# Performance work log

Measured on AMD Instinct MI355X. Metric: run time of the kernel, lower is better.

The kernel has to match this reference:

```python
import jax, jax.numpy as jnp
import numpy as np

B, S, F, H = 4, 1024, 512, 16
D = F // H  # head_dim = 32

def setup_inputs() -> dict:
    key = jax.random.key(0)
    ks = jax.random.split(key, 9)
    init = lambda k, shp: 0.1 * jax.random.normal(k, shp, dtype=jnp.float32)
    return {
        "kv": jax.random.normal(ks[0], (B, S, F), dtype=jnp.float32),
        "q": jax.random.normal(ks[1], (B, S, F), dtype=jnp.float32),
        "mask": jnp.ones((B, 1, S, S), dtype=jnp.int32),
        "Wq": init(ks[2], (F, F)),
        "Wk": init(ks[3], (F, F)),
        "Wv": init(ks[4], (F, F)),
        "Wo": init(ks[5], (F, F)),
        "rel_table": init(ks[6], (2 * S + 1, D)),  # nn.Embed(2*length_q+1, head_dim)
        "Wrel": init(ks[7], (D, D)),  # rel_pos_dense, no bias
    }

def reference(kv, q, mask, Wq, Wk, Wv, Wo, rel_table, Wrel):
    b, s, f = q.shape
    h, d = H, f // H
    qh = (q @ Wq).reshape(b, s, h, d)
    kh = (kv @ Wk).reshape(b, s, h, d)
    vh = (kv @ Wv).reshape(b, s, h, d)
    # raw content scores [b,h,q,k]
    scores = jnp.einsum('bqhd,bkhd->bhqk', qh, kh)
    # relative-position embedding: dist in [0, 2s], table lookup + dense
    dist = jnp.arange(s)[None, :] - jnp.arange(s)[:, None] + s  # [q,k]
    emb = rel_table[dist] @ Wrel  # [q,k,d]
    scores = scores + jnp.einsum('bqhd,qkd->bhqk', qh, emb)
    scores = scores / jnp.sqrt(jnp.asarray(d, scores.dtype))
    # mask-select before softmax (mask [b,1,q,k] broadcast over heads)
    scores = jnp.where(mask > 0, scores, -jnp.inf)
    attn = jax.nn.softmax(scores, axis=-1)
    out = jnp.einsum('bhqk,bkhd->bqhd', attn, vh).reshape(b, s, f)
    return out @ Wo  # dropout is identity (training=False)
```

## Files before the change

### kernel.cpp

```cpp
#include <hip/hip_runtime.h>

#define S_ 1024
#define H_ 16
#define D_ 32

typedef float f32x4 __attribute__((ext_vector_type(4)));
typedef short bf16x8 __attribute__((ext_vector_type(8)));
typedef unsigned long long u64;

static __device__ __forceinline__ short f2b(float f) {
    union { float f; unsigned u; } x; x.f = f;
    unsigned u = x.u;
    unsigned r = u + 0x7fffu + ((u >> 16) & 1u);
    return (short)(r >> 16);
}
static __device__ __forceinline__ unsigned pk_rne(float lo, float hi) {
    union { float f; unsigned u; } a, b; a.f = lo; b.f = hi;
    unsigned ul = a.u + 0x7fffu + ((a.u >> 16) & 1u);
    unsigned uh = b.u + 0x7fffu + ((b.u >> 16) & 1u);
    return __builtin_amdgcn_perm(uh, ul, 0x07060302u);
}
static __device__ __forceinline__ unsigned pk_trunc(float lo, float hi) {
    union { float f; unsigned u; } a, b; a.f = lo; b.f = hi;
    return __builtin_amdgcn_perm(b.u, a.u, 0x07060302u);
}
static __device__ __forceinline__ float bperm(int bidx, float v) {
    union { float f; int i; } x; x.f = v;
    x.i = __builtin_amdgcn_ds_bpermute(bidx, x.i);
    return x.f;
}
static __device__ __forceinline__ int stg64(int row, int c8) {
    return row * 72 + (c8 ^ ((row & 3) << 3));
}

__global__ __launch_bounds__(256)
void prep_kernel(const float* __restrict__ rt, short* __restrict__ relb,
                 const int* __restrict__ mask, u64* __restrict__ mbits,
                 const float* __restrict__ Wq, const float* __restrict__ Wk,
                 const float* __restrict__ Wv, const float* __restrict__ Wo,
                 short* __restrict__ Wt)
{
    __shared__ float ls[32][33];
    int bid = blockIdx.x, t = threadIdx.x;
    if (bid < 257) {
        int i = bid * 256 + t;
        if (i < 2049 * 32) relb[i] = f2b(rt[i]);
        return;
    }
    bid -= 257;
    if (bid < 4096) {
        #pragma unroll
        for (int j = 0; j < 4; ++j) {
            int i = bid * 1024 + j * 256 + t;
            u64 bal = __ballot(mask[i] > 0);
            if ((t & 63) == 0) mbits[i >> 6] = bal;
        }
        return;
    }
    bid -= 4096;
    int mat = bid >> 8, tl = bid & 255, ti = tl >> 4, tj = tl & 15;
    const float* W = (mat == 0) ? Wq : (mat == 1) ? Wk : (mat == 2) ? Wv : Wo;
    int r = t >> 3, c = (t & 7) * 4;
    float4 v = *(const float4*)(W + (long)(ti * 32 + r) * 512 + tj * 32 + c);
    ls[r][c] = v.x; ls[r][c + 1] = v.y; ls[r][c + 2] = v.z; ls[r][c + 3] = v.w;
    __syncthreads();
    int nl = t >> 3, kk = (t & 7) * 4;
    uint2 o = { pk_rne(ls[kk][nl], ls[kk + 1][nl]),
                pk_rne(ls[kk + 2][nl], ls[kk + 3][nl]) };
    *(uint2*)(Wt + ((long)mat * 512 + tj * 32 + nl) * 512 + ti * 32 + kk) = o;
}

__global__ __launch_bounds__(256)
void gemm3_kernel(const float* __restrict__ q, const float* __restrict__ kv,
                  const short* __restrict__ Wt,
                  short* __restrict__ qh, short* __restrict__ kh, short* __restrict__ vt,
                  float scale)
{
    __shared__ __align__(16) short a_s[64 * 72];
    __shared__ __align__(16) short b_s[64 * 72];
    const int t = threadIdx.x;
    const int w = t >> 6, lane = t & 63, l15 = lane & 15, quad = lane >> 4;
    const int wm = w & 1, wn = w >> 1;

    int bid = blockIdx.x;
    const int mat = bid >> 9;
    const int rr_ = bid & 511;
    const int bm = (rr_ & 63) * 64, bn = (rr_ >> 6) * 64;
    const float* A = (mat == 0) ? q : kv;
    const short* Wm = Wt + (long)mat * 262144;

    const int srow = t >> 2, scg = (t & 3) << 4;
    f32x4 acc[2][2] = {};

    for (int k0 = 0; k0 < 512; k0 += 64) {
        {
            const float* ap = A + (long)(bm + srow) * 512 + k0 + scg;
            float4 v0 = *(const float4*)(ap);
            float4 v1 = *(const float4*)(ap + 4);
            float4 v2 = *(const float4*)(ap + 8);
            float4 v3 = *(const float4*)(ap + 12);
            uint4 o0 = { pk_rne(v0.x, v0.y), pk_rne(v0.z, v0.w),
                         pk_rne(v1.x, v1.y), pk_rne(v1.z, v1.w) };
            uint4 o1 = { pk_rne(v2.x, v2.y), pk_rne(v2.z, v2.w),
                         pk_rne(v3.x, v3.y), pk_rne(v3.z, v3.w) };
            *(uint4*)(a_s + stg64(srow, scg)) = o0;
            *(uint4*)(a_s + stg64(srow, scg + 8)) = o1;
        }
        {
            const short* bp = Wm + (long)(bn + srow) * 512 + k0 + scg;
            *(bf16x8*)(b_s + stg64(srow, scg))     = *(const bf16x8*)(bp);
            *(bf16x8*)(b_s + stg64(srow, scg + 8)) = *(const bf16x8*)(bp + 8);
        }
        __syncthreads();
        bf16x8 af[2][2], bfr[2][2];
        #pragma unroll
        for (int i = 0; i < 2; ++i)
            #pragma unroll
            for (int ks = 0; ks < 2; ++ks) {
                af[i][ks]  = *(const bf16x8*)(a_s + stg64(wm * 32 + i * 16 + l15, ks * 32 + quad * 8));
                bfr[i][ks] = *(const bf16x8*)(b_s + stg64(wn * 32 + i * 16 + l15, ks * 32 + quad * 8));
            }
        if (mat == 2) {
            #pragma unroll
            for (int i = 0; i < 2; ++i)
                #pragma unroll
                for (int j = 0; j < 2; ++j)
                    #pragma unroll
                    for (int ks = 0; ks < 2; ++ks)
                        acc[i][j] = __builtin_amdgcn_mfma_f32_16x16x32_bf16(bfr[i][ks], af[j][ks], acc[i][j], 0, 0, 0);
        } else {
            #pragma unroll
            for (int i = 0; i < 2; ++i)
                #pragma unroll
                for (int j = 0; j < 2; ++j)
                    #pragma unroll
                    for (int ks = 0; ks < 2; ++ks)
                        acc[i][j] = __builtin_amdgcn_mfma_f32_16x16x32_bf16(af[i][ks], bfr[j][ks], acc[i][j], 0, 0, 0);
        }
        __syncthreads();
    }

    if (mat < 2) {
        short* out = (mat == 0) ? qh : kh;
        float alpha = (mat == 0) ? scale : 1.0f;
        #pragma unroll
        for (int i = 0; i < 2; ++i)
            #pragma unroll
            for (int j = 0; j < 2; ++j)
                #pragma unroll
                for (int r = 0; r < 4; ++r) {
                    int m = bm + wm * 32 + i * 16 + quad * 4 + r;
                    int n = bn + wn * 32 + j * 16 + l15;
                    int bb = m >> 10, s = m & 1023, hh = n >> 5, dd = n & 31;
                    out[((long)((bb * 16 + hh) * 1024 + s)) * 32 + dd] = f2b(acc[i][j][r] * alpha);
                }
    } else {
        #pragma unroll
        for (int i = 0; i < 2; ++i)
            #pragma unroll
            for (int j = 0; j < 2; ++j)
                #pragma unroll
                for (int r = 0; r < 4; ++r) {
                    int n = bn + wn * 32 + i * 16 + quad * 4 + r;
                    int m = bm + wm * 32 + j * 16 + l15;
                    int bb = m >> 10, s = m & 1023, hh = n >> 5, dd = n & 31;
                    int sp = (s & ~63) | ((s & 15) << 2) | ((s >> 4) & 3);
                    vt[((long)((bb * 16 + hh) * 32 + dd)) * 1024 + sp] = f2b(acc[i][j][r]);
                }
    }
}

__global__ __launch_bounds__(256)
void gemm_out_kernel(const short* __restrict__ ao, const short* __restrict__ Wt,
                     float* __restrict__ out)
{
    __shared__ __align__(16) short a_s[64 * 72];
    __shared__ __align__(16) short b_s[64 * 72];
    const int t = threadIdx.x;
    const int w = t >> 6, lane = t & 63, l15 = lane & 15, quad = lane >> 4;
    const int wm = w & 1, wn = w >> 1;
    const int bm = (blockIdx.x & 63) * 64, bn = (blockIdx.x >> 6) * 64;
    const short* Wm = Wt + (long)3 * 262144;
    const int srow = t >> 2, scg = (t & 3) << 4;
    f32x4 acc[2][2] = {};

    for (int k0 = 0; k0 < 512; k0 += 64) {
        {
            const short* apb = ao + (long)(bm + srow) * 512 + k0 + scg;
            *(bf16x8*)(a_s + stg64(srow, scg))     = *(const bf16x8*)(apb);
            *(bf16x8*)(a_s + stg64(srow, scg + 8)) = *(const bf16x8*)(apb + 8);
            const short* bpb = Wm + (long)(bn + srow) * 512 + k0 + scg;
            *(bf16x8*)(b_s + stg64(srow, scg))     = *(const bf16x8*)(bpb);
            *(bf16x8*)(b_s + stg64(srow, scg + 8)) = *(const bf16x8*)(bpb + 8);
        }
        __syncthreads();
        bf16x8 af[2][2], bfr[2][2];
        #pragma unroll
        for (int i = 0; i < 2; ++i)
            #pragma unroll
            for (int ks = 0; ks < 2; ++ks) {
                af[i][ks]  = *(const bf16x8*)(a_s + stg64(wm * 32 + i * 16 + l15, ks * 32 + quad * 8));
                bfr[i][ks] = *(const bf16x8*)(b_s + stg64(wn * 32 + i * 16 + l15, ks * 32 + quad * 8));
            }
        #pragma unroll
        for (int i = 0; i < 2; ++i)
            #pragma unroll
            for (int j = 0; j < 2; ++j)
                #pragma unroll
                for (int ks = 0; ks < 2; ++ks)
                    acc[i][j] = __builtin_amdgcn_mfma_f32_16x16x32_bf16(af[i][ks], bfr[j][ks], acc[i][j], 0, 0, 0);
        __syncthreads();
    }
    #pragma unroll
    for (int i = 0; i < 2; ++i)
        #pragma unroll
        for (int j = 0; j < 2; ++j)
            #pragma unroll
            for (int r = 0; r < 4; ++r) {
                int m = bm + wm * 32 + i * 16 + quad * 4 + r;
                int n = bn + wn * 32 + j * 16 + l15;
                out[(long)m * 512 + n] = acc[i][j][r];
            }
}

__global__ __launch_bounds__(256)
void attn_kernel(const short* __restrict__ qh, const float* __restrict__ wrel,
                 const short* __restrict__ kh, const short* __restrict__ vt,
                 const short* __restrict__ relb, const u64* __restrict__ mbits,
                 short* __restrict__ ao)
{
    __shared__ __align__(16) short smem[4 * 2 * 16 * 72];
    const int t = threadIdx.x;
    const int w = t >> 6, lane = t & 63, l15 = lane & 15, quad = lane >> 4;
    short* pw0 = smem + w * (2 * 16 * 72);
    short* pw1 = pw0 + 16 * 72;

    const int half = w & 1, qsel = w >> 1;
    const int gw = blockIdx.x * 2 + qsel;
    const int qt = gw & 63, h = (gw >> 6) & 15, b = gw >> 10;
    const int q0 = qt * 16, bh = b * H_ + h;
    const int c0 = half * 8;

    const long qbase = ((long)bh * S_ + q0 + l15) * D_ + quad * 8;
    const bf16x8 a_qh = *(const bf16x8*)(qh + qbase);
    const long kv_bh = (long)bh * S_ * D_;
    const u64* mrow = mbits + ((long)b * S_ + q0 + quad * 4) * 16;

    bf16x8 a_qr;
    {
        #pragma unroll
        for (int nt = 0; nt < 2; ++nt) {
            const float* wp = wrel + (long)(nt * 16 + l15) * 32 + quad * 8;
            float4 w0 = *(const float4*)(wp);
            float4 w1 = *(const float4*)(wp + 4);
            bf16x8 bw;
            *(uint4*)&bw = (uint4){ pk_rne(w0.x, w0.y), pk_rne(w0.z, w0.w),
                                    pk_rne(w1.x, w1.y), pk_rne(w1.z, w1.w) };
            f32x4 z = {0.f, 0.f, 0.f, 0.f};
            f32x4 cq = __builtin_amdgcn_mfma_f32_16x16x32_bf16(a_qh, bw, z, 0, 0, 0);
            #pragma unroll
            for (int r = 0; r < 4; ++r)
                pw0[(quad * 4 + r) * 36 + nt * 16 + l15] = f2b(cq[r]);
        }
        asm volatile("" ::: "memory");
        a_qr = *(const bf16x8*)(pw0 + l15 * 36 + quad * 8);
        asm volatile("" ::: "memory");
    }

    int bidx[4];
    #pragma unroll
    for (int r = 0; r < 4; ++r)
        bidx[r] = (quad * 16 + ((l15 + 15 - (quad * 4 + r)) & 15)) * 4;

    f32x4 oacc[2] = {};
    float l4[4] = {0.f, 0.f, 0.f, 0.f};

    bf16x8 preg0 = {}, preg1 = {};
    bf16x8 bv00 = {}, bv01 = {}, bv10 = {}, bv11 = {};

    for (int i = 0; i < 8; ++i) {
        const int c = c0 + i;
        const int kbase = c * 64;
        const int ub = kbase - q0 + (S_ - 15);
        short* pwbuf = (i & 1) ? pw1 : pw0;

        float bb[4][4];
        {
            f32x4 ctf[5];
            #pragma unroll
            for (int ut = 0; ut < 5; ++ut) {
                bf16x8 bre = *(const bf16x8*)(relb + (long)(ub + ut * 16 + l15) * D_ + quad * 8);
                f32x4 z = {0.f, 0.f, 0.f, 0.f};
                ctf[ut] = __builtin_amdgcn_mfma_f32_16x16x32_bf16(a_qr, bre, z, 0, 0, 0);
            }
            #pragma unroll
            for (int r = 0; r < 4; ++r) {
                int cnd = l15 > quad * 4 + r;
                float tt[5];
                #pragma unroll
                for (int ut = 0; ut < 5; ++ut) tt[ut] = bperm(bidx[r], ctf[ut][r]);
                bb[r][0] = cnd ? tt[1] : tt[0];
                bb[r][1] = cnd ? tt[2] : tt[1];
                bb[r][2] = cnd ? tt[3] : tt[2];
                bb[r][3] = cnd ? tt[4] : tt[3];
            }
        }
        f32x4 sc[4];
        #pragma unroll
        for (int kt = 0; kt < 4; ++kt) {
            bf16x8 bk = *(const bf16x8*)(kh + kv_bh + (long)(kbase + kt * 16 + l15) * D_ + quad * 8);
            f32x4 z = {0.f, 0.f, 0.f, 0.f};
            sc[kt] = __builtin_amdgcn_mfma_f32_16x16x32_bf16(a_qh, bk, z, 0, 0, 0);
        }
        if (i) {
            oacc[0] = __builtin_amdgcn_mfma_f32_16x16x32_bf16(preg0, bv00, oacc[0], 0, 0, 0);
            oacc[1] = __builtin_amdgcn_mfma_f32_16x16x32_bf16(preg0, bv01, oacc[1], 0, 0, 0);
            oacc[0] = __builtin_amdgcn_mfma_f32_16x16x32_bf16(preg1, bv10, oacc[0], 0, 0, 0);
            oacc[1] = __builtin_amdgcn_mfma_f32_16x16x32_bf16(preg1, bv11, oacc[1], 0, 0, 0);
        }
        bv00 = *(const bf16x8*)(vt + kv_bh + (long)(l15) * S_ + kbase + quad * 8);
        bv01 = *(const bf16x8*)(vt + kv_bh + (long)(16 + l15) * S_ + kbase + quad * 8);
        bv10 = *(const bf16x8*)(vt + kv_bh + (long)(l15) * S_ + kbase + 32 + quad * 8);
        bv11 = *(const bf16x8*)(vt + kv_bh + (long)(16 + l15) * S_ + kbase + 32 + quad * 8);

        #pragma unroll
        for (int r = 0; r < 4; ++r) {
            float s0 = sc[0][r] + bb[r][0];
            float s1 = sc[1][r] + bb[r][1];
            float s2 = sc[2][r] + bb[r][2];
            float s3 = sc[3][r] + bb[r][3];
            u64 mw = mrow[r * 16 + c] >> l15;
            unsigned lo = (unsigned)mw, hi = (unsigned)(mw >> 32);
            float p0 = __expf(s0); p0 = (lo & 1u)         ? p0 : 0.f;
            float p1 = __expf(s1); p1 = ((lo >> 16) & 1u) ? p1 : 0.f;
            float p2 = __expf(s2); p2 = (hi & 1u)         ? p2 : 0.f;
            float p3 = __expf(s3); p3 = ((hi >> 16) & 1u) ? p3 : 0.f;
            l4[r] += (p0 + p1) + (p2 + p3);
            u64 pv = ((u64)pk_trunc(p2, p3) << 32) | (u64)pk_trunc(p0, p1);
            *(u64*)(pwbuf + (quad * 4 + r) * 72 + l15 * 4) = pv;
        }
        asm volatile("" ::: "memory");
        preg0 = *(const bf16x8*)(pwbuf + l15 * 72 + quad * 8);
        preg1 = *(const bf16x8*)(pwbuf + l15 * 72 + 32 + quad * 8);
    }
    oacc[0] = __builtin_amdgcn_mfma_f32_16x16x32_bf16(preg0, bv00, oacc[0], 0, 0, 0);
    oacc[1] = __builtin_amdgcn_mfma_f32_16x16x32_bf16(preg0, bv01, oacc[1], 0, 0, 0);
    oacc[0] = __builtin_amdgcn_mfma_f32_16x16x32_bf16(preg1, bv10, oacc[0], 0, 0, 0);
    oacc[1] = __builtin_amdgcn_mfma_f32_16x16x32_bf16(preg1, bv11, oacc[1], 0, 0, 0);

    #pragma unroll
    for (int r = 0; r < 4; ++r) {
        float l = l4[r];
        l += __shfl_xor(l, 1, 64);
        l += __shfl_xor(l, 2, 64);
        l += __shfl_xor(l, 4, 64);
        l += __shfl_xor(l, 8, 64);
        l4[r] = l;
    }

    asm volatile("" ::: "memory");
    float* fo = (float*)pw0;
    float* fl = (float*)pw1;
    #pragma unroll
    for (int r = 0; r < 4; ++r) {
        #pragma unroll
        for (int dt = 0; dt < 2; ++dt)
            fo[(quad * 4 + r) * 32 + dt * 16 + l15] = oacc[dt][r];
        if (l15 == 0) fl[quad * 4 + r] = l4[r];
    }
    __syncthreads();
    if (half == 0) {
        const float* po = (const float*)(smem + (w ^ 1) * (2 * 16 * 72));
        const float* pl = po + 576;
        #pragma unroll
        for (int r = 0; r < 4; ++r) {
            int row = quad * 4 + r;
            float inv = 1.0f / (l4[r] + pl[row]);
            #pragma unroll
            for (int dt = 0; dt < 2; ++dt) {
                float o = oacc[dt][r] + po[row * 32 + dt * 16 + l15];
                ao[((long)(b * S_ + q0 + row) * H_ + h) * D_ + dt * 16 + l15] = f2b(o * inv);
            }
        }
    }
}

extern "C" void kernel_launch(void* const* d_in, const int* in_sizes, int n_in,
                              void* d_out, int out_size, void* d_ws, size_t ws_size,
                              hipStream_t stream) {
    (void)in_sizes; (void)n_in; (void)out_size; (void)ws_size;
    const float* kv   = (const float*)d_in[0];
    const float* q    = (const float*)d_in[1];
    const int*   mask = (const int*)d_in[2];
    const float* Wq   = (const float*)d_in[3];
    const float* Wk   = (const float*)d_in[4];
    const float* Wv   = (const float*)d_in[5];
    const float* Wo   = (const float*)d_in[6];
    const float* rt   = (const float*)d_in[7];
    const float* Wrel = (const float*)d_in[8];

    char* ws = (char*)d_ws;
    short* qh   = (short*)(ws);
    short* kh   = (short*)(ws + (4u  << 20));
    short* vt   = (short*)(ws + (8u  << 20));
    short* ao   = (short*)(ws + (12u << 20));
    short* Wt   = (short*)(ws + (16u << 20));
    short* relb = (short*)(ws + (18u << 20));
    u64*  mbits = (u64*) (ws + (18u << 20) + (256u << 10));

    const float scale = 0.17677669529663687f;

    prep_kernel<<<257 + 4096 + 1024, 256, 0, stream>>>(
        rt, relb, mask, mbits, Wq, Wk, Wv, Wo, Wt);

    gemm3_kernel<<<1536, 256, 0, stream>>>(q, kv, Wt, qh, kh, vt, scale);

    attn_kernel<<<2048, 256, 0, stream>>>(qh, Wrel, kh, vt, relb, mbits, ao);

    gemm_out_kernel<<<512, 256, 0, stream>>>(ao, Wt, (float*)d_out);
}
```

Baseline: 191.9 us.

## Remap attention blocks to XCDs by head and drop software-pipelined PV MMA

```diff
diff --git a/kernel.cpp b/kernel.cpp
--- a/kernel.cpp
+++ b/kernel.cpp
@@ -236,9 +236,12 @@
     short* pw1 = pw0 + 16 * 72;
 
     const int half = w & 1, qsel = w >> 1;
-    const int gw = blockIdx.x * 2 + qsel;
-    const int qt = gw & 63, h = (gw >> 6) & 15, b = gw >> 10;
-    const int q0 = qt * 16, bh = b * H_ + h;
+    const int bid = blockIdx.x;
+    const int xcd = bid & 7, loc = bid >> 3;
+    const int bh = xcd + 8 * (loc >> 5);
+    const int qt = (loc & 31) * 2 + qsel;
+    const int b = bh >> 4, h = bh & 15;
+    const int q0 = qt * 16;
     const int c0 = half * 8;
 
     const long qbase = ((long)bh * S_ + q0 + l15) * D_ + quad * 8;
@@ -275,9 +278,6 @@
     f32x4 oacc[2] = {};
     float l4[4] = {0.f, 0.f, 0.f, 0.f};
 
-    bf16x8 preg0 = {}, preg1 = {};
-    bf16x8 bv00 = {}, bv01 = {}, bv10 = {}, bv11 = {};
-
     for (int i = 0; i < 8; ++i) {
         const int c = c0 + i;
         const int kbase = c * 64;
@@ -312,16 +312,6 @@
             f32x4 z = {0.f, 0.f, 0.f, 0.f};
             sc[kt] = __builtin_amdgcn_mfma_f32_16x16x32_bf16(a_qh, bk, z, 0, 0, 0);
         }
-        if (i) {
-            oacc[0] = __builtin_amdgcn_mfma_f32_16x16x32_bf16(preg0, bv00, oacc[0], 0, 0, 0);
-            oacc[1] = __builtin_amdgcn_mfma_f32_16x16x32_bf16(preg0, bv01, oacc[1], 0, 0, 0);
-            oacc[0] = __builtin_amdgcn_mfma_f32_16x16x32_bf16(preg1, bv10, oacc[0], 0, 0, 0);
-            oacc[1] = __builtin_amdgcn_mfma_f32_16x16x32_bf16(preg1, bv11, oacc[1], 0, 0, 0);
-        }
-        bv00 = *(const bf16x8*)(vt + kv_bh + (long)(l15) * S_ + kbase + quad * 8);
-        bv01 = *(const bf16x8*)(vt + kv_bh + (long)(16 + l15) * S_ + kbase + quad * 8);
-        bv10 = *(const bf16x8*)(vt + kv_bh + (long)(l15) * S_ + kbase + 32 + quad * 8);
-        bv11 = *(const bf16x8*)(vt + kv_bh + (long)(16 + l15) * S_ + kbase + 32 + quad * 8);
 
         #pragma unroll
         for (int r = 0; r < 4; ++r) {
@@ -340,13 +330,19 @@
             *(u64*)(pwbuf + (quad * 4 + r) * 72 + l15 * 4) = pv;
         }
         asm volatile("" ::: "memory");
-        preg0 = *(const bf16x8*)(pwbuf + l15 * 72 + quad * 8);
-        preg1 = *(const bf16x8*)(pwbuf + l15 * 72 + 32 + quad * 8);
-    }
-    oacc[0] = __builtin_amdgcn_mfma_f32_16x16x32_bf16(preg0, bv00, oacc[0], 0, 0, 0);
-    oacc[1] = __builtin_amdgcn_mfma_f32_16x16x32_bf16(preg0, bv01, oacc[1], 0, 0, 0);
-    oacc[0] = __builtin_amdgcn_mfma_f32_16x16x32_bf16(preg1, bv10, oacc[0], 0, 0, 0);
-    oacc[1] = __builtin_amdgcn_mfma_f32_16x16x32_bf16(preg1, bv11, oacc[1], 0, 0, 0);
+        {
+            bf16x8 p0r = *(const bf16x8*)(pwbuf + l15 * 72 + quad * 8);
+            bf16x8 p1r = *(const bf16x8*)(pwbuf + l15 * 72 + 32 + quad * 8);
+            bf16x8 v00 = *(const bf16x8*)(vt + kv_bh + (long)(l15) * S_ + kbase + quad * 8);
+            bf16x8 v01 = *(const bf16x8*)(vt + kv_bh + (long)(16 + l15) * S_ + kbase + quad * 8);
+            bf16x8 v10 = *(const bf16x8*)(vt + kv_bh + (long)(l15) * S_ + kbase + 32 + quad * 8);
+            bf16x8 v11 = *(const bf16x8*)(vt + kv_bh + (long)(16 + l15) * S_ + kbase + 32 + quad * 8);
+            oacc[0] = __builtin_amdgcn_mfma_f32_16x16x32_bf16(p0r, v00, oacc[0], 0, 0, 0);
+            oacc[1] = __builtin_amdgcn_mfma_f32_16x16x32_bf16(p0r, v01, oacc[1], 0, 0, 0);
+            oacc[0] = __builtin_amdgcn_mfma_f32_16x16x32_bf16(p1r, v10, oacc[0], 0, 0, 0);
+            oacc[1] = __builtin_amdgcn_mfma_f32_16x16x32_bf16(p1r, v11, oacc[1], 0, 0, 0);
+        }
+    }
 
     #pragma unroll
     for (int r = 0; r < 4; ++r) {
```

After: 201.7 us. +5.1%, slower.
